# Optimization experiments

Hardware: AMD Instinct MI355X
Metric: run time of the kernel (lower is better)

The kernel has to match this reference:

```python
import jax, jax.numpy as jnp
import numpy as np

N = 100000   # nodes
E = 1200000  # edges
D = 64       # input_dim
H = 64       # hidden_dim
L = 4        # num_layers (GIN layers)
G = 128      # graphs in batch
BN_EPS = 1e-5


def setup_inputs() -> dict:
    key = jax.random.key(0)
    ks = jax.random.split(key, 8)
    x = jax.random.normal(ks[0], (N, D), dtype=jnp.float32)
    edge_index = jax.random.randint(ks[1], (2, E), 0, N)
    batch = jnp.sort(jax.random.randint(ks[2], (N,), 0, G))
    s = 1.0 / np.sqrt(H).astype(np.float32)
    W_emb = jax.random.normal(ks[3], (D, H), dtype=jnp.float32) * s
    b_emb = jnp.zeros((H,), jnp.float32)
    W1 = jax.random.normal(ks[4], (L, H, H), dtype=jnp.float32) * s
    b1 = jnp.zeros((L, H), jnp.float32)
    gamma = jnp.ones((L, H), jnp.float32)
    beta = jnp.zeros((L, H), jnp.float32)
    W2 = jax.random.normal(ks[5], (L, H, H), dtype=jnp.float32) * s
    b2 = jnp.zeros((L, H), jnp.float32)
    return dict(x=x, edge_index=edge_index, batch=batch, W_emb=W_emb, b_emb=b_emb,
                W1=W1, b1=b1, gamma=gamma, beta=beta, W2=W2, b2=b2)


def _mean_pool(h, batch):
    # global_mean_pool: segment sum / segment count, fixed num_segments=G
    s = jax.ops.segment_sum(h, batch, num_segments=G)
    cnt = jax.ops.segment_sum(jnp.ones((h.shape[0],), h.dtype), batch, num_segments=G)
    return s / jnp.maximum(cnt, 1.0)[:, None]


def _bn(h, g, b):
    # BatchNorm1d in training mode: batch statistics, biased variance
    mu = h.mean(axis=0)
    var = h.var(axis=0)
    return g * (h - mu) * jax.lax.rsqrt(var + BN_EPS) + b


def reference(x, edge_index, batch, W_emb, b_emb, W1, b1, gamma, beta, W2, b2):
    src, dst = edge_index[0], edge_index[1]
    h = x @ W_emb + b_emb                      # [N, H] embedding_h
    reps = [_mean_pool(h, batch)]
    for i in range(L):
        # GINConv, eps=0: mlp((1+eps)*x + sum_{j in N(i)} x_j)
        agg = jax.ops.segment_sum(h[src], dst, num_segments=N)
        z = h + agg
        # 2-layer MLP: Linear -> BN -> ReLU -> Linear
        z = jax.nn.relu(_bn(z @ W1[i] + b1[i], gamma[i], beta[i]))
        h = z @ W2[i] + b2[i]
        reps.append(_mean_pool(h, batch))
    return jnp.concatenate(reps, axis=1)       # [G, H*(L+1)]
```

## Files before the change

### kernel.cpp

```cpp
#include <hip/hip_runtime.h>
#include <hip/hip_bf16.h>

typedef __hip_bfloat16 bf16;
typedef unsigned short u16;
typedef unsigned int u32;
typedef __attribute__((ext_vector_type(8))) short short8;
typedef __attribute__((ext_vector_type(8))) unsigned short ushort8;
typedef __attribute__((ext_vector_type(4))) float f32x4;

#define N_NODES 100000
#define N_EDGES 1200000
#define DIM 64
#define NG 128
#define NLAYERS 4
#define BN_EPS 1e-5f

#define BKT_BITS 9
#define BKT 512
#define NBKT ((N_NODES + BKT - 1) / BKT)
#define SCAT_BLK 128
#define SCAT_CH ((N_EDGES + SCAT_BLK - 1) / SCAT_BLK)
#define CSR_CAP 8192

#define WS_GSUM   0
#define WS_GSUMSQ 64
#define WS_AB     128
#define WS_FLAG   256
#define WS_GB     320
#define WS_WALL   512
#define OFF_WEMB  0
#define OFF_BEMB  4096
#define OFF_W1    4160
#define OFF_B1    20544
#define OFF_GAMMA 20800
#define OFF_BETA  21056
#define OFF_W2    21312
#define OFF_B2    37696
#define W_TOTAL   37952
#define WS_PACC8  38464
#define WS_WPK    104000
#define WS_CUR    204000
#define WS_ROWPTR 304128
#define WS_CSR    404160
#define WS_Z      1604160
#define WS_H      4804160
#define WS_PAIR   8004160
#define WS_END    9204160
#define WS_NEED_BYTES ((size_t)WS_END * 4)

#define NBLK   ((N_NODES + 63) / 64)

__device__ __forceinline__ float b2f(bf16 v) { return __bfloat162float(v); }
__device__ __forceinline__ float us2f(unsigned short u) {
    return __uint_as_float(((u32)u) << 16);
}
__device__ __forceinline__ short f2bs(float f) {
    bf16 b = __float2bfloat16(f);
    u16 u; __builtin_memcpy(&u, &b, 2);
    return (short)u;
}

__device__ __forceinline__ float loadf(const void* p, long i, int flag) {
    if (flag) return ((const float*)p)[i];
    u32 w = ((u32)((const u16*)p)[i]) << 16;
    return __uint_as_float(w);
}

__global__ void k_diag(u32* out, float val) {
    if (threadIdx.x == 0 && blockIdx.x == 0) {
        bf16 b = __float2bfloat16(val);
        u16 bits;
        __builtin_memcpy(&bits, &b, 2);
        u32 w = ((u32)bits << 16) | bits;
        for (int i = 0; i < 8; i++) out[i] = w;
    }
}

__global__ void k_detect(const void* x, int* flag) {
    if (threadIdx.x == 0 && blockIdx.x == 0) {
        const u16* u = (const u16*)x;
        int bad = 0;
        for (int i = 0; i < 512; i++) {
            float v = __uint_as_float(((u32)u[i]) << 16);
            if (!(fabsf(v) < 100.f)) bad++;
        }
        *flag = (bad > 16) ? 1 : 0;
    }
}

__global__ __launch_bounds__(256) void k_convert(const void* W_emb, const void* b_emb,
                                                 const void* W1, const void* b1,
                                                 const void* gamma, const void* beta,
                                                 const void* W2, const void* b2,
                                                 const int* flagp, float* dst) {
    int f = *flagp;
    for (int i = blockIdx.x * blockDim.x + threadIdx.x; i < W_TOTAL;
         i += gridDim.x * blockDim.x) {
        const void* p; int off;
        if (i < OFF_BEMB)       { p = W_emb; off = i; }
        else if (i < OFF_W1)    { p = b_emb; off = i - OFF_BEMB; }
        else if (i < OFF_B1)    { p = W1;    off = i - OFF_W1; }
        else if (i < OFF_GAMMA) { p = b1;    off = i - OFF_B1; }
        else if (i < OFF_BETA)  { p = gamma; off = i - OFF_GAMMA; }
        else if (i < OFF_W2)    { p = beta;  off = i - OFF_BETA; }
        else if (i < OFF_B2)    { p = W2;    off = i - OFF_W2; }
        else                    { p = b2;    off = i - OFF_B2; }
        dst[i] = loadf(p, off, f);
    }
}

__global__ __launch_bounds__(256) void k_pack(const float* __restrict__ wall,
                                              u16* __restrict__ wpk) {
    int i = blockIdx.x * 256 + threadIdx.x;
    if (i >= 9 * 4096) return;
    int m = i >> 12, r = i & 4095;
    int j = r & 7, l = (r >> 3) & 63, cc = (r >> 9) & 3, kk = r >> 11;
    int d = kk * 32 + ((l >> 4) << 3) + j;
    int c = cc * 16 + (l & 15);
    int moff = (m == 0) ? OFF_WEMB
             : (m <= 4 ? OFF_W1 + (m - 1) * 4096 : OFF_W2 + (m - 5) * 4096);
    wpk[i] = (u16)f2bs(wall[moff + d * 64 + c]);
}

__global__ void k_gbounds(const int* __restrict__ batch, int* __restrict__ gb) {
    int t = threadIdx.x;
    if (t <= NG) {
        int a = 0, b = N_NODES;
        while (a < b) { int m = (a + b) >> 1; if (batch[m] < t) a = m + 1; else b = m; }
        gb[t] = a;
    }
}


__global__ __launch_bounds__(256) void k_bhist(const int* __restrict__ ei,
                                               int* __restrict__ bhist) {
    __shared__ int hl[NBKT];
    int tid = threadIdx.x;
    for (int b = tid; b < NBKT; b += 256) hl[b] = 0;
    __syncthreads();
    for (int e = blockIdx.x * 256 + tid; e < N_EDGES; e += gridDim.x * 256)
        atomicAdd(&hl[ei[N_EDGES + e] >> BKT_BITS], 1);
    __syncthreads();
    for (int b = tid; b < NBKT; b += 256)
        if (hl[b]) atomicAdd(&bhist[b], hl[b]);
}

__global__ __launch_bounds__(256) void k_bscan(const int* __restrict__ bhist,
                                               int* __restrict__ boff,
                                               int* __restrict__ bcur) {
    __shared__ int s[256];
    int tid = threadIdx.x;
    int v = (tid < NBKT) ? bhist[tid] : 0;
    s[tid] = v;
    __syncthreads();
    for (int off = 1; off < 256; off <<= 1) {
        int t = (tid >= off) ? s[tid - off] : 0;
        __syncthreads();
        s[tid] += t;
        __syncthreads();
    }
    if (tid < NBKT) { int e = s[tid] - v; boff[tid] = e; bcur[tid] = e; }
    if (tid == 0) boff[NBKT] = s[255];
}

__global__ __launch_bounds__(256) void k_bscatter(const int* __restrict__ ei,
                                                  int* __restrict__ bcur,
                                                  u32* __restrict__ pair) {
    __shared__ int cnt[NBKT];
    int tid = threadIdx.x;
    int cbeg = blockIdx.x * SCAT_CH;
    int cend = cbeg + SCAT_CH; if (cend > N_EDGES) cend = N_EDGES;
    for (int b = tid; b < NBKT; b += 256) cnt[b] = 0;
    __syncthreads();
    for (int e = cbeg + tid; e < cend; e += 256)
        atomicAdd(&cnt[ei[N_EDGES + e] >> BKT_BITS], 1);
    __syncthreads();
    for (int b = tid; b < NBKT; b += 256) {
        int c = cnt[b];
        cnt[b] = c ? atomicAdd(&bcur[b], c) : 0;
    }
    __syncthreads();
    for (int e = cbeg + tid; e < cend; e += 256) {
        int s = ei[e];
        int d = ei[N_EDGES + e];
        int pos = atomicAdd(&cnt[d >> BKT_BITS], 1);
        pair[pos] = (u32)s | ((u32)(d & (BKT - 1)) << 17);
    }
}

__global__ __launch_bounds__(256) void k_bcsr(const u32* __restrict__ pair,
                                              const int* __restrict__ boff,
                                              int* __restrict__ rowptr,
                                              int* __restrict__ csr) {
    __shared__ int degl[BKT];
    __shared__ int offl[BKT];
    __shared__ int sc[256];
    __shared__ int csrl[CSR_CAP];
    int b = blockIdx.x, tid = threadIdx.x;
    int nbase = b << BKT_BITS;
    int nodes = N_NODES - nbase; if (nodes > BKT) nodes = BKT;
    int p0 = boff[b], p1 = boff[b + 1];
    int span = p1 - p0;
    for (int i = tid; i < BKT; i += 256) degl[i] = 0;
    __syncthreads();
    for (int p = p0 + tid; p < p1; p += 256)
        atomicAdd(&degl[pair[p] >> 17], 1);
    __syncthreads();
    int a0 = degl[2 * tid], a1 = degl[2 * tid + 1];
    sc[tid] = a0 + a1;
    __syncthreads();
    for (int off = 1; off < 256; off <<= 1) {
        int t = (tid >= off) ? sc[tid - off] : 0;
        __syncthreads();
        sc[tid] += t;
        __syncthreads();
    }
    int base = sc[tid] - (a0 + a1);
    offl[2 * tid] = base;
    offl[2 * tid + 1] = base + a0;
    __syncthreads();
    for (int i = tid; i < nodes; i += 256) rowptr[nbase + i] = p0 + offl[i];
    if (b == NBKT - 1 && tid == 0) rowptr[N_NODES] = p1;
    for (int i = tid; i < BKT; i += 256) degl[i] = offl[i];
    __syncthreads();
    if (span <= CSR_CAP) {
        for (int p = p0 + tid; p < p1; p += 256) {
            u32 pk = pair[p];
            int pos = atomicAdd(&degl[pk >> 17], 1);
            csrl[pos] = (int)(pk & 0x1FFFFu);
        }
        __syncthreads();
        for (int i = tid; i < span; i += 256) csr[p0 + i] = csrl[i];
    } else {
        for (int p = p0 + tid; p < p1; p += 256) {
            u32 pk = pair[p];
            int pos = atomicAdd(&degl[pk >> 17], 1);
            csr[p0 + pos] = (int)(pk & 0x1FFFFu);
        }
    }
}

__device__ __forceinline__ void store_tile(u16* cb, const f32x4* acc, bf16* out,
                                           int base, int wv, int lane) {
    int r15 = lane & 15, half = lane >> 4;
#pragma unroll
    for (int cc = 0; cc < 4; cc++) {
#pragma unroll
        for (int r = 0; r < 4; r++) {
            int trow = half * 4 + r;
            int idx = (trow * 64 + cc * 16 + r15) ^ ((trow & 7) << 3);
            cb[idx] = (u16)f2bs(acc[cc][r]);
        }
    }
#pragma unroll
    for (int p = 0; p < 2; p++) {
        int trow = lane >> 2;
        int o = (trow * 64 + (lane & 3) * 8 + p * 32) ^ ((trow & 7) << 3);
        short8 val = *(const short8*)&cb[o];
        int grow = base + (wv << 4) + trow;
        if (grow < N_NODES)
            *(short8*)((u16*)out + (long)grow * 64 + (lane & 3) * 8 + p * 32) = val;
    }
}

__global__ __launch_bounds__(256) void k_embed(const void* __restrict__ x,
                                               const int* __restrict__ flagp,
                                               const u16* __restrict__ wpk,
                                               const float* __restrict__ bf_,
                                               bf16* __restrict__ h) {
    __shared__ u16 cbuf[4 * 1024];
    int tid = threadIdx.x, lane = tid & 63, wv = tid >> 6;
    int r15 = lane & 15, half = lane >> 4;
    int f = *flagp;
    int base = blockIdx.x * 64;
    int row = base + (wv << 4) + r15;
    bool valid = row < N_NODES;

    float xv[16];
#pragma unroll
    for (int j = 0; j < 16; j++) xv[j] = 0.f;
    if (valid) {
        if (f) {
            const f32x4* xp = (const f32x4*)((const float*)x + (long)row * 64 + half * 8);
            f32x4 u0 = xp[0], u1 = xp[1], w0 = xp[8], w1 = xp[9];
#pragma unroll
            for (int j = 0; j < 4; j++) {
                xv[j] = u0[j]; xv[4 + j] = u1[j];
                xv[8 + j] = w0[j]; xv[12 + j] = w1[j];
            }
        } else {
            const ushort8* xp = (const ushort8*)((const u16*)x + (long)row * 64 + half * 8);
            ushort8 s0 = xp[0], s1 = xp[4];
#pragma unroll
            for (int j = 0; j < 8; j++) { xv[j] = us2f(s0[j]); xv[8 + j] = us2f(s1[j]); }
        }
    }
    short8 A0, A1;
#pragma unroll
    for (int j = 0; j < 8; j++) { A0[j] = f2bs(xv[j]); A1[j] = f2bs(xv[8 + j]); }

    const short8* Wp = (const short8*)wpk;
    short8 Bw[8];
#pragma unroll
    for (int i = 0; i < 8; i++) Bw[i] = Wp[i * 64 + lane];
    f32x4 acc[4];
#pragma unroll
    for (int cc = 0; cc < 4; cc++) {
        float bb = bf_[cc * 16 + r15];
        acc[cc] = (f32x4){bb, bb, bb, bb};
        acc[cc] = __builtin_amdgcn_mfma_f32_16x16x32_bf16(A0, Bw[cc], acc[cc], 0, 0, 0);
        acc[cc] = __builtin_amdgcn_mfma_f32_16x16x32_bf16(A1, Bw[4 + cc], acc[cc], 0, 0, 0);
    }
    store_tile(cbuf + wv * 1024, acc, h, base, wv, lane);
}

__global__ __launch_bounds__(256) void k_layer1(const bf16* __restrict__ h,
                                                const int* __restrict__ rowptr,
                                                const int* __restrict__ csr,
                                                bf16* __restrict__ z,
                                                const u16* __restrict__ wpk,
                                                const float* __restrict__ bf_,
                                                float* __restrict__ gsum,
                                                float* __restrict__ gsumsq) {
    __shared__ u16 cbuf[4 * 1024];
    __shared__ float psum[DIM], psq[DIM];
    int tid = threadIdx.x, lane = tid & 63, wv = tid >> 6;
    int r15 = lane & 15, half = lane >> 4;
    int base = blockIdx.x * 64;
    int row = base + (wv << 4) + r15;
    bool valid = row < N_NODES;

    if (tid < DIM) { psum[tid] = 0.f; psq[tid] = 0.f; }
    __syncthreads();

    float v[16];
#pragma unroll
    for (int j = 0; j < 16; j++) v[j] = 0.f;
    int p0 = 0, dg = 0;
    if (valid) {
        p0 = rowptr[row];
        dg = rowptr[row + 1] - p0;
        const ushort8* hp = (const ushort8*)((const u16*)h + (long)row * 64 + half * 8);
        ushort8 s0 = hp[0], s1 = hp[4];
#pragma unroll
        for (int j = 0; j < 8; j++) { v[j] = us2f(s0[j]); v[8 + j] = us2f(s1[j]); }
    }
    const int* cp = csr + p0;
    int t = 0;
    int n0 = 0, n1 = 0, n2 = 0, n3 = 0;
    if (4 <= dg) { n0 = cp[0]; n1 = cp[1]; n2 = cp[2]; n3 = cp[3]; }
    while (t + 4 <= dg) {
        const ushort8* q0 = (const ushort8*)((const u16*)h + (long)n0 * 64 + half * 8);
        const ushort8* q1 = (const ushort8*)((const u16*)h + (long)n1 * 64 + half * 8);
        const ushort8* q2 = (const ushort8*)((const u16*)h + (long)n2 * 64 + half * 8);
        const ushort8* q3 = (const ushort8*)((const u16*)h + (long)n3 * 64 + half * 8);
        ushort8 a0 = q0[0], b0 = q0[4];
        ushort8 a1 = q1[0], b1 = q1[4];
        ushort8 a2 = q2[0], b2 = q2[4];
        ushort8 a3 = q3[0], b3 = q3[4];
        t += 4;
        if (t + 4 <= dg) { n0 = cp[t]; n1 = cp[t + 1]; n2 = cp[t + 2]; n3 = cp[t + 3]; }
#pragma unroll
        for (int j = 0; j < 8; j++) {
            v[j]     += (us2f(a0[j]) + us2f(a1[j])) + (us2f(a2[j]) + us2f(a3[j]));
            v[8 + j] += (us2f(b0[j]) + us2f(b1[j])) + (us2f(b2[j]) + us2f(b3[j]));
        }
    }
    for (; t < dg; t++) {
        int s = cp[t];
        const ushort8* q = (const ushort8*)((const u16*)h + (long)s * 64 + half * 8);
        ushort8 a = q[0], b = q[4];
#pragma unroll
        for (int j = 0; j < 8; j++) { v[j] += us2f(a[j]); v[8 + j] += us2f(b[j]); }
    }

    short8 A0, A1;
#pragma unroll
    for (int j = 0; j < 8; j++) { A0[j] = f2bs(v[j]); A1[j] = f2bs(v[8 + j]); }

    const short8* Wp = (const short8*)wpk;
    short8 Bw[8];
#pragma unroll
    for (int i = 0; i < 8; i++) Bw[i] = Wp[i * 64 + lane];
    f32x4 acc[4];
#pragma unroll
    for (int cc = 0; cc < 4; cc++) {
        float bb = bf_[cc * 16 + r15];
        acc[cc] = (f32x4){bb, bb, bb, bb};
        acc[cc] = __builtin_amdgcn_mfma_f32_16x16x32_bf16(A0, Bw[cc], acc[cc], 0, 0, 0);
        acc[cc] = __builtin_amdgcn_mfma_f32_16x16x32_bf16(A1, Bw[4 + cc], acc[cc], 0, 0, 0);
    }

#pragma unroll
    for (int cc = 0; cc < 4; cc++) {
        float s = 0.f, q = 0.f;
#pragma unroll
        for (int r = 0; r < 4; r++) {
            int grow = base + (wv << 4) + half * 4 + r;
            if (grow < N_NODES) { float val = acc[cc][r]; s += val; q += val * val; }
        }
        s += __shfl_xor(s, 16, 64); s += __shfl_xor(s, 32, 64);
        q += __shfl_xor(q, 16, 64); q += __shfl_xor(q, 32, 64);
        if (half == 0) {
            atomicAdd(&psum[cc * 16 + r15], s);
            atomicAdd(&psq[cc * 16 + r15], q);
        }
    }

    store_tile(cbuf + wv * 1024, acc, z, base, wv, lane);

    __syncthreads();
    if (tid < DIM) {
        atomicAdd(&gsum[tid], psum[tid]);
        atomicAdd(&gsumsq[tid], psq[tid]);
    }
}

__global__ void k_stats(const float* __restrict__ gsum, const float* __restrict__ gsumsq,
                        const float* __restrict__ gamma_f, const float* __restrict__ beta_f,
                        float* __restrict__ ab) {
    int c = threadIdx.x;
    if (c < DIM) {
        float inv_n = 1.0f / (float)N_NODES;
        float mu = gsum[c] * inv_n;
        float var = fmaxf(gsumsq[c] * inv_n - mu * mu, 0.f);
        float a = gamma_f[c] * rsqrtf(var + BN_EPS);
        ab[c] = a;
        ab[DIM + c] = beta_f[c] - mu * a;
    }
}

__global__ __launch_bounds__(256) void k_gemm2(const bf16* __restrict__ z,
                                               bf16* __restrict__ h,
                                               const u16* __restrict__ wpk,
                                               const float* __restrict__ bf_,
                                               const float* __restrict__ ab) {
    __shared__ u16 cbuf[4 * 1024];
    int tid = threadIdx.x, lane = tid & 63, wv = tid >> 6;
    int r15 = lane & 15, half = lane >> 4;
    int base = blockIdx.x * 64;
    int row = base + (wv << 4) + r15;
    bool valid = row < N_NODES;

    const f32x4* ap = (const f32x4*)ab;
    f32x4 A0v = ap[half * 2], A1v = ap[half * 2 + 1];
    f32x4 A2v = ap[8 + half * 2], A3v = ap[8 + half * 2 + 1];
    f32x4 S0v = ap[16 + half * 2], S1v = ap[16 + half * 2 + 1];
    f32x4 S2v = ap[24 + half * 2], S3v = ap[24 + half * 2 + 1];

    float xv[16];
#pragma unroll
    for (int j = 0; j < 16; j++) xv[j] = 0.f;
    if (valid) {
        const ushort8* zp = (const ushort8*)((const u16*)z + (long)row * 64 + half * 8);
        ushort8 s0 = zp[0], s1 = zp[4];
#pragma unroll
        for (int j = 0; j < 4; j++) {
            xv[j]      = fmaxf(A0v[j] * us2f(s0[j])     + S0v[j], 0.f);
            xv[4 + j]  = fmaxf(A1v[j] * us2f(s0[4 + j]) + S1v[j], 0.f);
            xv[8 + j]  = fmaxf(A2v[j] * us2f(s1[j])     + S2v[j], 0.f);
            xv[12 + j] = fmaxf(A3v[j] * us2f(s1[4 + j]) + S3v[j], 0.f);
        }
    }
    short8 A0, A1;
#pragma unroll
    for (int j = 0; j < 8; j++) { A0[j] = f2bs(xv[j]); A1[j] = f2bs(xv[8 + j]); }

    const short8* Wp = (const short8*)wpk;
    short8 Bw[8];
#pragma unroll
    for (int i = 0; i < 8; i++) Bw[i] = Wp[i * 64 + lane];
    f32x4 acc[4];
#pragma unroll
    for (int cc = 0; cc < 4; cc++) {
        float bb = bf_[cc * 16 + r15];
        acc[cc] = (f32x4){bb, bb, bb, bb};
        acc[cc] = __builtin_amdgcn_mfma_f32_16x16x32_bf16(A0, Bw[cc], acc[cc], 0, 0, 0);
        acc[cc] = __builtin_amdgcn_mfma_f32_16x16x32_bf16(A1, Bw[4 + cc], acc[cc], 0, 0, 0);
    }
    store_tile(cbuf + wv * 1024, acc, h, base, wv, lane);
}

__global__ __launch_bounds__(256) void k_pool2(const bf16* __restrict__ h,
                                               const int* __restrict__ gb,
                                               float* __restrict__ pacc8) {
    __shared__ float ps[4][DIM];
    int g = blockIdx.x >> 3, sl = blockIdx.x & 7;
    int tid = threadIdx.x, lane = tid & 63, wv = tid >> 6;
    int chunk = lane & 7, rg = lane >> 3;
    int lo = gb[g], hi = gb[g + 1];
    float acc[8];
#pragma unroll
    for (int j = 0; j < 8; j++) acc[j] = 0.f;
    for (int r = lo + (sl * 4 + wv) * 8 + rg; r < hi; r += 256) {
        ushort8 d = *(const ushort8*)((const u16*)h + (long)r * 64 + chunk * 8);
#pragma unroll
        for (int j = 0; j < 8; j++) acc[j] += us2f(d[j]);
    }
#pragma unroll
    for (int j = 0; j < 8; j++) {
        acc[j] += __shfl_xor(acc[j], 8, 64);
        acc[j] += __shfl_xor(acc[j], 16, 64);
        acc[j] += __shfl_xor(acc[j], 32, 64);
    }
    if (rg == 0) {
#pragma unroll
        for (int j = 0; j < 8; j++) ps[wv][chunk * 8 + j] = acc[j];
    }
    __syncthreads();
    if (tid < DIM)
        pacc8[((long)g * 8 + sl) * DIM + tid] =
            ps[0][tid] + ps[1][tid] + ps[2][tid] + ps[3][tid];
}

__global__ void k_poolw(const float* __restrict__ pacc8, const int* __restrict__ gb,
                        void* __restrict__ out, int rep, const int* __restrict__ flagp) {
    int g = blockIdx.x, c = threadIdx.x;
    int f = *flagp;
    float tot = 0.f;
#pragma unroll
    for (int sl = 0; sl < 8; sl++) tot += pacc8[((long)g * 8 + sl) * DIM + c];
    tot /= fmaxf((float)(gb[g + 1] - gb[g]), 1.f);
    long idx = (long)g * (DIM * (NLAYERS + 1)) + rep * DIM + c;
    if (f) ((float*)out)[idx] = tot;
    else   ((bf16*)out)[idx] = __float2bfloat16(tot);
}

extern "C" void kernel_launch(void* const* d_in, const int* in_sizes, int n_in,
                              void* d_out, int out_size, void* d_ws, size_t ws_size,
                              hipStream_t stream) {
    static const int EXPECT[11] = {6400000, 2400000, 100000, 4096, 64,
                                   16384, 256, 256, 256, 16384, 256};
    int bad = (n_in == 11) ? -1 : 99;
    if (bad < 0)
        for (int i = 0; i < 11; i++)
            if (in_sizes[i] != EXPECT[i]) { bad = i; break; }
    if (bad >= 0) {
        k_diag<<<1, 64, 0, stream>>>((u32*)d_out, 3000.0f + 100.0f * (float)bad);
        return;
    }
    if (ws_size < WS_NEED_BYTES) {
        k_diag<<<1, 64, 0, stream>>>((u32*)d_out, 1000.0f + (float)(ws_size >> 20));
        return;
    }

    const void* x     = d_in[0];
    const int*  ei    = (const int*)d_in[1];
    const int*  batch = (const int*)d_in[2];

    float* ws = (float*)d_ws;
    float* gsum   = ws + WS_GSUM;
    float* gsumsq = ws + WS_GSUMSQ;
    float* ab     = ws + WS_AB;
    int*   flagp  = (int*)(ws + WS_FLAG);
    int*   gb     = (int*)(ws + WS_GB);
    float* WALL   = ws + WS_WALL;
    float* pacc8  = ws + WS_PACC8;
    u16*   wpk    = (u16*)(ws + WS_WPK);
    int*   curr   = (int*)(ws + WS_CUR);
    int*   bhist  = curr;
    int*   boff   = curr + 256;
    int*   bcur   = curr + 512;
    int*   rowptr = (int*)(ws + WS_ROWPTR);
    int*   csr    = (int*)(ws + WS_CSR);
    u32*   pair   = (u32*)(ws + WS_PAIR);
    bf16*  z      = (bf16*)(ws + WS_Z);
    bf16*  h      = (bf16*)(ws + WS_H);

    k_detect<<<1, 64, 0, stream>>>(x, flagp);
    k_convert<<<64, 256, 0, stream>>>(d_in[3], d_in[4], d_in[5], d_in[6],
                                      d_in[7], d_in[8], d_in[9], d_in[10], flagp, WALL);
    k_pack<<<144, 256, 0, stream>>>(WALL, wpk);
    k_gbounds<<<1, 256, 0, stream>>>(batch, gb);

    hipMemsetAsync(bhist, 0, NBKT * sizeof(int), stream);
    k_bhist<<<256, 256, 0, stream>>>(ei, bhist);
    k_bscan<<<1, 256, 0, stream>>>(bhist, boff, bcur);
    k_bscatter<<<SCAT_BLK, 256, 0, stream>>>(ei, bcur, pair);
    k_bcsr<<<NBKT, 256, 0, stream>>>(pair, boff, rowptr, csr);

    k_embed<<<NBLK, 256, 0, stream>>>(x, flagp, wpk, WALL + OFF_BEMB, h);
    k_pool2<<<NG * 8, 256, 0, stream>>>(h, gb, pacc8);
    k_poolw<<<NG, 64, 0, stream>>>(pacc8, gb, d_out, 0, flagp);
    for (int l = 0; l < NLAYERS; l++) {
        hipMemsetAsync(gsum, 0, 128 * sizeof(float), stream);
        k_layer1<<<NBLK, 256, 0, stream>>>(h, rowptr, csr, z,
                                           wpk + (1 + l) * 4096,
                                           WALL + OFF_B1 + l * DIM, gsum, gsumsq);
        k_stats<<<1, 64, 0, stream>>>(gsum, gsumsq, WALL + OFF_GAMMA + l * DIM,
                                      WALL + OFF_BETA + l * DIM, ab);
        k_gemm2<<<NBLK, 256, 0, stream>>>(z, h, wpk + (5 + l) * 4096,
                                          WALL + OFF_B2 + l * DIM, ab);
        k_pool2<<<NG * 8, 256, 0, stream>>>(h, gb, pacc8);
        k_poolw<<<NG, 64, 0, stream>>>(pacc8, gb, d_out, l + 1, flagp);
    }
}
```

Before: 496.4 us.

## Fuse mean pooling into GEMM epilogues and BN stats into layer kernel

Mean-pool accumulation moves into the epilogues of the embedding and second-GEMM kernels, which add fp32 accumulators to a per-graph buffer with atomics. This removes the separate pool kernel that re-read h. BN statistics finalization moves into the last block of k_layer1 through a completion counter, and the per-layer memset is dropped in favour of zeroing inside k_poolw. The neighbour gather loop is unrolled to 8 loads in flight. The cost is heavy atomic contention on the 128×64 pooling buffer, and the pool now sums fp32 values instead of rounded bf16 ones.

Result: slower. 806.7 us (+62.5%).

```diff
diff --git a/kernel.cpp b/kernel.cpp
--- a/kernel.cpp
+++ b/kernel.cpp
@@ -24,10 +24,12 @@
 
 #define WS_GSUM   0
 #define WS_GSUMSQ 64
-#define WS_AB     128
-#define WS_FLAG   256
-#define WS_GB     320
-#define WS_WALL   512
+#define WS_CNT    128
+#define WS_AB     192
+#define WS_FLAG   320
+#define WS_GB     384
+#define WS_PACC   576
+#define WS_WALL   8768
 #define OFF_WEMB  0
 #define OFF_BEMB  4096
 #define OFF_W1    4160
@@ -37,20 +39,18 @@
 #define OFF_W2    21312
 #define OFF_B2    37696
 #define W_TOTAL   37952
-#define WS_PACC8  38464
-#define WS_WPK    104000
-#define WS_CUR    204000
-#define WS_ROWPTR 304128
-#define WS_CSR    404160
-#define WS_Z      1604160
-#define WS_H      4804160
-#define WS_PAIR   8004160
-#define WS_END    9204160
+#define WS_WPK    46720
+#define WS_CUR    65152
+#define WS_ROWPTR 66176
+#define WS_CSR    166208
+#define WS_Z      1366208
+#define WS_H      4566208
+#define WS_PAIR   7766208
+#define WS_END    8966208
 #define WS_NEED_BYTES ((size_t)WS_END * 4)
 
 #define NBLK   ((N_NODES + 63) / 64)
 
-__device__ __forceinline__ float b2f(bf16 v) { return __bfloat162float(v); }
 __device__ __forceinline__ float us2f(unsigned short u) {
     return __uint_as_float(((u32)u) << 16);
 }
@@ -263,18 +263,48 @@
     }
 }
 
+__device__ __forceinline__ void pool_accum(const f32x4* acc, const int* gl,
+                                           float* pacc, int base, int wv, int lane) {
+    int r15 = lane & 15, half = lane >> 4;
+    int lr0 = (wv << 4) + half * 4;
+    int grow0 = base + lr0;
+    if (grow0 + 3 < N_NODES && gl[lr0] == gl[lr0 + 3]) {
+        int g0 = gl[lr0];
+#pragma unroll
+        for (int cc = 0; cc < 4; cc++)
+            atomicAdd(&pacc[(long)g0 * DIM + cc * 16 + r15],
+                      (acc[cc][0] + acc[cc][1]) + (acc[cc][2] + acc[cc][3]));
+        return;
+    }
+#pragma unroll
+    for (int r = 0; r < 4; r++) {
+        if (grow0 + r < N_NODES) {
+            int g = gl[lr0 + r];
+#pragma unroll
+            for (int cc = 0; cc < 4; cc++)
+                atomicAdd(&pacc[(long)g * DIM + cc * 16 + r15], acc[cc][r]);
+        }
+    }
+}
+
 __global__ __launch_bounds__(256) void k_embed(const void* __restrict__ x,
                                                const int* __restrict__ flagp,
                                                const u16* __restrict__ wpk,
                                                const float* __restrict__ bf_,
-                                               bf16* __restrict__ h) {
+                                               bf16* __restrict__ h,
+                                               const int* __restrict__ batch,
+                                               float* __restrict__ pacc) {
     __shared__ u16 cbuf[4 * 1024];
+    __shared__ int gl[64];
     int tid = threadIdx.x, lane = tid & 63, wv = tid >> 6;
     int r15 = lane & 15, half = lane >> 4;
     int f = *flagp;
     int base = blockIdx.x * 64;
     int row = base + (wv << 4) + r15;
     bool valid = row < N_NODES;
+
+    if (tid < 64) { int rr = base + tid; gl[tid] = (rr < N_NODES) ? batch[rr] : 0; }
+    __syncthreads();
 
     float xv[16];
 #pragma unroll
@@ -312,7 +342,13 @@
         acc[cc] = __builtin_amdgcn_mfma_f32_16x16x32_bf16(A1, Bw[4 + cc], acc[cc], 0, 0, 0);
     }
     store_tile(cbuf + wv * 1024, acc, h, base, wv, lane);
-}
+    pool_accum(acc, gl, pacc, base, wv, lane);
+}
+
+#define GLD(n, aV, bV) { const ushort8* q = (const ushort8*)(hc + (long)(n) * 64); \
+                         aV = q[0]; bV = q[4]; }
+#define ACC2(aa, bb) { _Pragma("unroll") \
+    for (int j = 0; j < 8; j++) { v[j] += us2f(aa[j]); v[8 + j] += us2f(bb[j]); } }
 
 __global__ __launch_bounds__(256) void k_layer1(const bf16* __restrict__ h,
                                                 const int* __restrict__ rowptr,
@@ -321,9 +357,14 @@
                                                 const u16* __restrict__ wpk,
                                                 const float* __restrict__ bf_,
                                                 float* __restrict__ gsum,
-                                                float* __restrict__ gsumsq) {
+                                                float* __restrict__ gsumsq,
+                                                int* __restrict__ cntp,
+                                                const float* __restrict__ gamma_f,
+                                                const float* __restrict__ beta_f,
+                                                float* __restrict__ ab) {
     __shared__ u16 cbuf[4 * 1024];
     __shared__ float psum[DIM], psq[DIM];
+    __shared__ int lastf;
     int tid = threadIdx.x, lane = tid & 63, wv = tid >> 6;
     int r15 = lane & 15, half = lane >> 4;
     int base = blockIdx.x * 64;
@@ -346,32 +387,44 @@
         for (int j = 0; j < 8; j++) { v[j] = us2f(s0[j]); v[8 + j] = us2f(s1[j]); }
     }
     const int* cp = csr + p0;
+    const u16* hc = (const u16*)h + half * 8;
     int t = 0;
-    int n0 = 0, n1 = 0, n2 = 0, n3 = 0;
-    if (4 <= dg) { n0 = cp[0]; n1 = cp[1]; n2 = cp[2]; n3 = cp[3]; }
-    while (t + 4 <= dg) {
-        const ushort8* q0 = (const ushort8*)((const u16*)h + (long)n0 * 64 + half * 8);
-        const ushort8* q1 = (const ushort8*)((const u16*)h + (long)n1 * 64 + half * 8);
-        const ushort8* q2 = (const ushort8*)((const u16*)h + (long)n2 * 64 + half * 8);
-        const ushort8* q3 = (const ushort8*)((const u16*)h + (long)n3 * 64 + half * 8);
-        ushort8 a0 = q0[0], b0 = q0[4];
-        ushort8 a1 = q1[0], b1 = q1[4];
-        ushort8 a2 = q2[0], b2 = q2[4];
-        ushort8 a3 = q3[0], b3 = q3[4];
+    int m0 = 0, m1 = 0, m2 = 0, m3 = 0, m4 = 0, m5 = 0, m6 = 0, m7 = 0;
+    if (8 <= dg) {
+        m0 = cp[0]; m1 = cp[1]; m2 = cp[2]; m3 = cp[3];
+        m4 = cp[4]; m5 = cp[5]; m6 = cp[6]; m7 = cp[7];
+    }
+    while (t + 8 <= dg) {
+        ushort8 a0, b0, a1, b1, a2, b2, a3, b3, a4, b4, a5, b5, a6, b6, a7, b7;
+        GLD(m0, a0, b0); GLD(m1, a1, b1); GLD(m2, a2, b2); GLD(m3, a3, b3);
+        GLD(m4, a4, b4); GLD(m5, a5, b5); GLD(m6, a6, b6); GLD(m7, a7, b7);
+        t += 8;
+        if (t + 8 <= dg) {
+            m0 = cp[t];     m1 = cp[t + 1]; m2 = cp[t + 2]; m3 = cp[t + 3];
+            m4 = cp[t + 4]; m5 = cp[t + 5]; m6 = cp[t + 6]; m7 = cp[t + 7];
+        }
+        ACC2(a0, b0); ACC2(a1, b1); ACC2(a2, b2); ACC2(a3, b3);
+        ACC2(a4, b4); ACC2(a5, b5); ACC2(a6, b6); ACC2(a7, b7);
+    }
+    if (t + 4 <= dg) {
+        int j0 = cp[t], j1 = cp[t + 1], j2 = cp[t + 2], j3 = cp[t + 3];
+        ushort8 a0, b0, a1, b1, a2, b2, a3, b3;
+        GLD(j0, a0, b0); GLD(j1, a1, b1); GLD(j2, a2, b2); GLD(j3, a3, b3);
         t += 4;
-        if (t + 4 <= dg) { n0 = cp[t]; n1 = cp[t + 1]; n2 = cp[t + 2]; n3 = cp[t + 3]; }
-#pragma unroll
-        for (int j = 0; j < 8; j++) {
-            v[j]     += (us2f(a0[j]) + us2f(a1[j])) + (us2f(a2[j]) + us2f(a3[j]));
-            v[8 + j] += (us2f(b0[j]) + us2f(b1[j])) + (us2f(b2[j]) + us2f(b3[j]));
-        }
-    }
-    for (; t < dg; t++) {
-        int s = cp[t];
-        const ushort8* q = (const ushort8*)((const u16*)h + (long)s * 64 + half * 8);
-        ushort8 a = q[0], b = q[4];
-#pragma unroll
-        for (int j = 0; j < 8; j++) { v[j] += us2f(a[j]); v[8 + j] += us2f(b[j]); }
+        ACC2(a0, b0); ACC2(a1, b1); ACC2(a2, b2); ACC2(a3, b3);
+    }
+    if (t + 2 <= dg) {
+        int j0 = cp[t], j1 = cp[t + 1];
+        ushort8 a0, b0, a1, b1;
+        GLD(j0, a0, b0); GLD(j1, a1, b1);
+        t += 2;
+        ACC2(a0, b0); ACC2(a1, b1);
+    }
+    if (t < dg) {
+        int j0 = cp[t];
+        ushort8 a0, b0;
+        GLD(j0, a0, b0);
+        ACC2(a0, b0);
     }
 
     short8 A0, A1;
@@ -414,19 +467,21 @@
         atomicAdd(&gsum[tid], psum[tid]);
         atomicAdd(&gsumsq[tid], psq[tid]);
     }
-}
-
-__global__ void k_stats(const float* __restrict__ gsum, const float* __restrict__ gsumsq,
-                        const float* __restrict__ gamma_f, const float* __restrict__ beta_f,
-                        float* __restrict__ ab) {
-    int c = threadIdx.x;
-    if (c < DIM) {
+    __syncthreads();
+    if (tid == 0) {
+        __threadfence();
+        lastf = (atomicAdd(cntp, 1) == (int)gridDim.x - 1);
+    }
+    __syncthreads();
+    if (lastf && tid < DIM) {
+        float s = atomicAdd(&gsum[tid], 0.f);
+        float q = atomicAdd(&gsumsq[tid], 0.f);
         float inv_n = 1.0f / (float)N_NODES;
-        float mu = gsum[c] * inv_n;
-        float var = fmaxf(gsumsq[c] * inv_n - mu * mu, 0.f);
-        float a = gamma_f[c] * rsqrtf(var + BN_EPS);
-        ab[c] = a;
-        ab[DIM + c] = beta_f[c] - mu * a;
+        float mu = s * inv_n;
+        float var = fmaxf(q * inv_n - mu * mu, 0.f);
+        float a = gamma_f[tid] * rsqrtf(var + BN_EPS);
+        ab[tid] = a;
+        ab[DIM + tid] = beta_f[tid] - mu * a;
     }
 }
 
@@ -434,14 +489,20 @@
                                                bf16* __restrict__ h,
                                                const u16* __restrict__ wpk,
                                                const float* __restrict__ bf_,
-                                               const float* __restrict__ ab) {
+                                               const float* __restrict__ ab,
+                                               const int* __restrict__ batch,
+                                               float* __restrict__ pacc) {
     __shared__ u16 cbuf[4 * 1024];
+    __shared__ int gl[64];
     int tid = threadIdx.x, lane = tid & 63, wv = tid >> 6;
     int r15 = lane & 15, half = lane >> 4;
     int base = blockIdx.x * 64;
     int row = base + (wv << 4) + r15;
     bool valid = row < N_NODES;
 
+    if (tid < 64) { int rr = base + tid; gl[tid] = (rr < N_NODES) ? batch[rr] : 0; }
+    __syncthreads();
+
     const f32x4* ap = (const f32x4*)ab;
     f32x4 A0v = ap[half * 2], A1v = ap[half * 2 + 1];
     f32x4 A2v = ap[8 + half * 2], A3v = ap[8 + half * 2 + 1];
@@ -479,51 +540,26 @@
         acc[cc] = __builtin_amdgcn_mfma_f32_16x16x32_bf16(A1, Bw[4 + cc], acc[cc], 0, 0, 0);
     }
     store_tile(cbuf + wv * 1024, acc, h, base, wv, lane);
-}
-
-__global__ __launch_bounds__(256) void k_pool2(const bf16* __restrict__ h,
-                                               const int* __restrict__ gb,
-                                               float* __restrict__ pacc8) {
-    __shared__ float ps[4][DIM];
-    int g = blockIdx.x >> 3, sl = blockIdx.x & 7;
-    int tid = threadIdx.x, lane = tid & 63, wv = tid >> 6;
-    int chunk = lane & 7, rg = lane >> 3;
-    int lo = gb[g], hi = gb[g + 1];
-    float acc[8];
-#pragma unroll
-    for (int j = 0; j < 8; j++) acc[j] = 0.f;
-    for (int r = lo + (sl * 4 + wv) * 8 + rg; r < hi; r += 256) {
-        ushort8 d = *(const ushort8*)((const u16*)h + (long)r * 64 + chunk * 8);
-#pragma unroll
-        for (int j = 0; j < 8; j++) acc[j] += us2f(d[j]);
-    }
-#pragma unroll
-    for (int j = 0; j < 8; j++) {
-        acc[j] += __shfl_xor(acc[j], 8, 64);
-        acc[j] += __shfl_xor(acc[j], 16, 64);
-        acc[j] += __shfl_xor(acc[j], 32, 64);
-    }
-    if (rg == 0) {
-#pragma unroll
-        for (int j = 0; j < 8; j++) ps[wv][chunk * 8 + j] = acc[j];
-    }
-    __syncthreads();
-    if (tid < DIM)
-        pacc8[((long)g * 8 + sl) * DIM + tid] =
-            ps[0][tid] + ps[1][tid] + ps[2][tid] + ps[3][tid];
-}
-
-__global__ void k_poolw(const float* __restrict__ pacc8, const int* __restrict__ gb,
-                        void* __restrict__ out, int rep, const int* __restrict__ flagp) {
+    pool_accum(acc, gl, pacc, base, wv, lane);
+}
+
+__global__ void k_poolw(float* __restrict__ pacc, const int* __restrict__ gb,
+                        void* __restrict__ out, int rep, const int* __restrict__ flagp,
+                        float* __restrict__ gsum, float* __restrict__ gsumsq,
+                        int* __restrict__ cntp) {
     int g = blockIdx.x, c = threadIdx.x;
     int f = *flagp;
-    float tot = 0.f;
-#pragma unroll
-    for (int sl = 0; sl < 8; sl++) tot += pacc8[((long)g * 8 + sl) * DIM + c];
+    float tot = pacc[(long)g * DIM + c];
+    pacc[(long)g * DIM + c] = 0.f;
     tot /= fmaxf((float)(gb[g + 1] - gb[g]), 1.f);
     long idx = (long)g * (DIM * (NLAYERS + 1)) + rep * DIM + c;
     if (f) ((float*)out)[idx] = tot;
     else   ((bf16*)out)[idx] = __float2bfloat16(tot);
+    if (g == 0) {
+        gsum[c] = 0.f;
+        gsumsq[c] = 0.f;
+        if (c == 0) *cntp = 0;
+    }
 }
 
 extern "C" void kernel_launch(void* const* d_in, const int* in_sizes, int n_in,
@@ -551,11 +587,12 @@
     float* ws = (float*)d_ws;
     float* gsum   = ws + WS_GSUM;
     float* gsumsq = ws + WS_GSUMSQ;
+    int*   cntp   = (int*)(ws + WS_CNT);
     float* ab     = ws + WS_AB;
     int*   flagp  = (int*)(ws + WS_FLAG);
     int*   gb     = (int*)(ws + WS_GB);
+    float* pacc   = ws + WS_PACC;
     float* WALL   = ws + WS_WALL;
-    float* pacc8  = ws + WS_PACC8;
     u16*   wpk    = (u16*)(ws + WS_WPK);
     int*   curr   = (int*)(ws + WS_CUR);
     int*   bhist  = curr;
@@ -567,6 +604,7 @@
     bf16*  z      = (bf16*)(ws + WS_Z);
     bf16*  h      = (bf16*)(ws + WS_H);
 
+    hipMemsetAsync(ws, 0, (size_t)(WS_WALL) * 4, stream);
     k_detect<<<1, 64, 0, stream>>>(x, flagp);
     k_convert<<<64, 256, 0, stream>>>(d_in[3], d_in[4], d_in[5], d_in[6],
                                       d_in[7], d_in[8], d_in[9], d_in[10], flagp, WALL);
@@ -579,19 +617,17 @@
     k_bscatter<<<SCAT_BLK, 256, 0, stream>>>(ei, bcur, pair);
     k_bcsr<<<NBKT, 256, 0, stream>>>(pair, boff, rowptr, csr);
 
-    k_embed<<<NBLK, 256, 0, stream>>>(x, flagp, wpk, WALL + OFF_BEMB, h);
-    k_pool2<<<NG * 8, 256, 0, stream>>>(h, gb, pacc8);
-    k_poolw<<<NG, 64, 0, stream>>>(pacc8, gb, d_out, 0, flagp);
+    k_embed<<<NBLK, 256, 0, stream>>>(x, flagp, wpk, WALL + OFF_BEMB, h, batch, pacc);
+    k_poolw<<<NG, 64, 0, stream>>>(pacc, gb, d_out, 0, flagp, gsum, gsumsq, cntp);
     for (int l = 0; l < NLAYERS; l++) {
-        hipMemsetAsync(gsum, 0, 128 * sizeof(float), stream);
         k_layer1<<<NBLK, 256, 0, stream>>>(h, rowptr, csr, z,
                                            wpk + (1 + l) * 4096,
-                                           WALL + OFF_B1 + l * DIM, gsum, gsumsq);
-        k_stats<<<1, 64, 0, stream>>>(gsum, gsumsq, WALL + OFF_GAMMA + l * DIM,
-                                      WALL + OFF_BETA + l * DIM, ab);
+                                           WALL + OFF_B1 + l * DIM, gsum, gsumsq, cntp,
+                                           WALL + OFF_GAMMA + l * DIM,
+                                           WALL + OFF_BETA + l * DIM, ab);
         k_gemm2<<<NBLK, 256, 0, stream>>>(z, h, wpk + (5 + l) * 4096,
-                                          WALL + OFF_B2 + l * DIM, ab);
-        k_pool2<<<NG * 8, 256, 0, stream>>>(h, gb, pacc8);
-        k_poolw<<<NG, 64, 0, stream>>>(pacc8, gb, d_out, l + 1, flagp);
-    }
-}
+                                          WALL + OFF_B2 + l * DIM, ab, batch, pacc);
+        k_poolw<<<NG, 64, 0, stream>>>(pacc, gb, d_out, l + 1, flagp,
+                                       gsum, gsumsq, cntp);
+    }
+}
```

## Process nodes in degree-sorted order in layer aggregation kernel

Applied to the files above, without the earlier changes.

Adds a counting sort of nodes by in-degree (histogram, scan, fill) that builds a permutation, reusing the pair buffer for storage. The aggregation+GEMM kernel then handles nodes in permuted order, so each wavefront gets rows of similar degree and the gather loops diverge less. Output rows are scattered back to their original positions. The cost is three extra small kernels plus less coalesced row reads and writes of h and z.

New measurement: 496.1 us. Within noise of the previous version (-0.1%).

```diff
diff --git a/kernel.cpp b/kernel.cpp
--- a/kernel.cpp
+++ b/kernel.cpp
@@ -50,7 +50,6 @@
 
 #define NBLK   ((N_NODES + 63) / 64)
 
-__device__ __forceinline__ float b2f(bf16 v) { return __bfloat162float(v); }
 __device__ __forceinline__ float us2f(unsigned short u) {
     return __uint_as_float(((u32)u) << 16);
 }
@@ -240,6 +239,66 @@
     }
 }
 
+
+__global__ __launch_bounds__(256) void k_deghist(const int* __restrict__ rowptr,
+                                                 int* __restrict__ dhist) {
+    __shared__ int hl[256];
+    int tid = threadIdx.x;
+    hl[tid] = 0;
+    __syncthreads();
+    for (int i = blockIdx.x * 256 + tid; i < N_NODES; i += gridDim.x * 256) {
+        int d = rowptr[i + 1] - rowptr[i];
+        int b = 255 - (d > 255 ? 255 : d);
+        atomicAdd(&hl[b], 1);
+    }
+    __syncthreads();
+    if (hl[tid]) atomicAdd(&dhist[tid], hl[tid]);
+}
+
+__global__ void k_degscan(const int* __restrict__ dhist, int* __restrict__ dhcur,
+                          int* __restrict__ perm) {
+    __shared__ int s[256];
+    int tid = threadIdx.x;
+    int v = dhist[tid];
+    s[tid] = v;
+    __syncthreads();
+    for (int off = 1; off < 256; off <<= 1) {
+        int t = (tid >= off) ? s[tid - off] : 0;
+        __syncthreads();
+        s[tid] += t;
+        __syncthreads();
+    }
+    dhcur[tid] = s[tid] - v;
+    if (tid < NBLK * 64 - N_NODES) perm[N_NODES + tid] = N_NODES;
+}
+
+__global__ __launch_bounds__(256) void k_degfill(const int* __restrict__ rowptr,
+                                                 int* __restrict__ dhcur,
+                                                 int* __restrict__ perm) {
+    __shared__ int cnt[256];
+    int tid = threadIdx.x;
+    int chunk = (N_NODES + gridDim.x - 1) / gridDim.x;
+    int beg = blockIdx.x * chunk;
+    int end = beg + chunk; if (end > N_NODES) end = N_NODES;
+    cnt[tid] = 0;
+    __syncthreads();
+    for (int i = beg + tid; i < end; i += 256) {
+        int d = rowptr[i + 1] - rowptr[i];
+        int b = 255 - (d > 255 ? 255 : d);
+        atomicAdd(&cnt[b], 1);
+    }
+    __syncthreads();
+    int c = cnt[tid];
+    cnt[tid] = c ? atomicAdd(&dhcur[tid], c) : 0;
+    __syncthreads();
+    for (int i = beg + tid; i < end; i += 256) {
+        int d = rowptr[i + 1] - rowptr[i];
+        int b = 255 - (d > 255 ? 255 : d);
+        int pos = atomicAdd(&cnt[b], 1);
+        perm[pos] = i;
+    }
+}
+
 __device__ __forceinline__ void store_tile(u16* cb, const f32x4* acc, bf16* out,
                                            int base, int wv, int lane) {
     int r15 = lane & 15, half = lane >> 4;
@@ -258,6 +317,29 @@
         int o = (trow * 64 + (lane & 3) * 8 + p * 32) ^ ((trow & 7) << 3);
         short8 val = *(const short8*)&cb[o];
         int grow = base + (wv << 4) + trow;
+        if (grow < N_NODES)
+            *(short8*)((u16*)out + (long)grow * 64 + (lane & 3) * 8 + p * 32) = val;
+    }
+}
+
+__device__ __forceinline__ void store_tile_p(u16* cb, const f32x4* acc, bf16* out,
+                                             const int* pl, int wv, int lane) {
+    int r15 = lane & 15, half = lane >> 4;
+#pragma unroll
+    for (int cc = 0; cc < 4; cc++) {
+#pragma unroll
+        for (int r = 0; r < 4; r++) {
+            int trow = half * 4 + r;
+            int idx = (trow * 64 + cc * 16 + r15) ^ ((trow & 7) << 3);
+            cb[idx] = (u16)f2bs(acc[cc][r]);
+        }
+    }
+#pragma unroll
+    for (int p = 0; p < 2; p++) {
+        int trow = lane >> 2;
+        int o = (trow * 64 + (lane & 3) * 8 + p * 32) ^ ((trow & 7) << 3);
+        short8 val = *(const short8*)&cb[o];
+        int grow = pl[(wv << 4) + trow];
         if (grow < N_NODES)
             *(short8*)((u16*)out + (long)grow * 64 + (lane & 3) * 8 + p * 32) = val;
     }
@@ -317,6 +399,7 @@
 __global__ __launch_bounds__(256) void k_layer1(const bf16* __restrict__ h,
                                                 const int* __restrict__ rowptr,
                                                 const int* __restrict__ csr,
+                                                const int* __restrict__ perm,
                                                 bf16* __restrict__ z,
                                                 const u16* __restrict__ wpk,
                                                 const float* __restrict__ bf_,
@@ -324,14 +407,17 @@
                                                 float* __restrict__ gsumsq) {
     __shared__ u16 cbuf[4 * 1024];
     __shared__ float psum[DIM], psq[DIM];
+    __shared__ int pl[64];
     int tid = threadIdx.x, lane = tid & 63, wv = tid >> 6;
     int r15 = lane & 15, half = lane >> 4;
     int base = blockIdx.x * 64;
-    int row = base + (wv << 4) + r15;
+
+    if (tid < DIM) { psum[tid] = 0.f; psq[tid] = 0.f; }
+    if (tid < 64) pl[tid] = perm[base + tid];
+    __syncthreads();
+
+    int row = pl[(wv << 4) + r15];
     bool valid = row < N_NODES;
-
-    if (tid < DIM) { psum[tid] = 0.f; psq[tid] = 0.f; }
-    __syncthreads();
 
     float v[16];
 #pragma unroll
@@ -396,8 +482,8 @@
         float s = 0.f, q = 0.f;
 #pragma unroll
         for (int r = 0; r < 4; r++) {
-            int grow = base + (wv << 4) + half * 4 + r;
-            if (grow < N_NODES) { float val = acc[cc][r]; s += val; q += val * val; }
+            int prow = pl[(wv << 4) + half * 4 + r];
+            if (prow < N_NODES) { float val = acc[cc][r]; s += val; q += val * val; }
         }
         s += __shfl_xor(s, 16, 64); s += __shfl_xor(s, 32, 64);
         q += __shfl_xor(q, 16, 64); q += __shfl_xor(q, 32, 64);
@@ -407,7 +493,7 @@
         }
     }
 
-    store_tile(cbuf + wv * 1024, acc, z, base, wv, lane);
+    store_tile_p(cbuf + wv * 1024, acc, z, pl, wv, lane);
 
     __syncthreads();
     if (tid < DIM) {
@@ -561,9 +647,12 @@
     int*   bhist  = curr;
     int*   boff   = curr + 256;
     int*   bcur   = curr + 512;
+    int*   dhist  = curr + 768;
+    int*   dhcur  = curr + 1024;
     int*   rowptr = (int*)(ws + WS_ROWPTR);
     int*   csr    = (int*)(ws + WS_CSR);
     u32*   pair   = (u32*)(ws + WS_PAIR);
+    int*   perm   = (int*)(ws + WS_PAIR);
     bf16*  z      = (bf16*)(ws + WS_Z);
     bf16*  h      = (bf16*)(ws + WS_H);
 
@@ -573,18 +662,22 @@
     k_pack<<<144, 256, 0, stream>>>(WALL, wpk);
     k_gbounds<<<1, 256, 0, stream>>>(batch, gb);
 
-    hipMemsetAsync(bhist, 0, NBKT * sizeof(int), stream);
+    hipMemsetAsync(curr, 0, 1280 * sizeof(int), stream);
     k_bhist<<<256, 256, 0, stream>>>(ei, bhist);
     k_bscan<<<1, 256, 0, stream>>>(bhist, boff, bcur);
     k_bscatter<<<SCAT_BLK, 256, 0, stream>>>(ei, bcur, pair);
     k_bcsr<<<NBKT, 256, 0, stream>>>(pair, boff, rowptr, csr);
+
+    k_deghist<<<128, 256, 0, stream>>>(rowptr, dhist);
+    k_degscan<<<1, 256, 0, stream>>>(dhist, dhcur, perm);
+    k_degfill<<<128, 256, 0, stream>>>(rowptr, dhcur, perm);
 
     k_embed<<<NBLK, 256, 0, stream>>>(x, flagp, wpk, WALL + OFF_BEMB, h);
     k_pool2<<<NG * 8, 256, 0, stream>>>(h, gb, pacc8);
     k_poolw<<<NG, 64, 0, stream>>>(pacc8, gb, d_out, 0, flagp);
     for (int l = 0; l < NLAYERS; l++) {
         hipMemsetAsync(gsum, 0, 128 * sizeof(float), stream);
-        k_layer1<<<NBLK, 256, 0, stream>>>(h, rowptr, csr, z,
+        k_layer1<<<NBLK, 256, 0, stream>>>(h, rowptr, csr, perm, z,
                                            wpk + (1 + l) * 4096,
                                            WALL + OFF_B1 + l * DIM, gsum, gsumsq);
         k_stats<<<1, 64, 0, stream>>>(gsum, gsumsq, WALL + OFF_GAMMA + l * DIM,
```
